# Optimization experiments

Hardware: AMD Instinct MI355X
Metric: run time of the kernel (lower is better)

The kernel has to match this reference:

```python
import jax, jax.numpy as jnp
import numpy as np

B, Q, K, H = 8, 512, 512, 64
KEY_D, QUERY_D, VAL_D = 256, 256, 256

def setup_inputs() -> dict:
    key = jax.random.key(0)
    ks = jax.random.split(key, 6)
    return {
        "key": jax.random.normal(ks[0], (B, K, KEY_D), dtype=jnp.float32),
        "query": jax.random.normal(ks[1], (B, Q, QUERY_D), dtype=jnp.float32),
        "value": jax.random.normal(ks[2], (B, K, VAL_D), dtype=jnp.float32),
        "mask": jnp.zeros((B, Q, K), dtype=bool),
        "W_k": jax.random.normal(ks[3], (KEY_D, H), dtype=jnp.float32) / np.sqrt(KEY_D),
        "W_q": jax.random.normal(ks[4], (QUERY_D, H), dtype=jnp.float32) / np.sqrt(QUERY_D),
        "w_v": jax.random.normal(ks[5], (H,), dtype=jnp.float32) / np.sqrt(H),
    }

def reference(key, query, value, mask, W_k, W_q, w_v):
    q = query @ W_q                      # [B, Q, H]
    k = key @ W_k                        # [B, K, H]
    feats = jnp.tanh(q[:, :, None, :] + k[:, None, :, :])  # [B, Q, K, H]
    score = jnp.einsum('bqkh,h->bqk', feats, w_v)           # [B, Q, K]
    score = jnp.where(mask, -jnp.inf, score)
    attn = jax.nn.softmax(score, axis=-1)                   # [B, Q, K]
    return jnp.einsum('bqk,bkd->bqd', attn, value)          # [B, Q, VAL_D]
```

## Files before the change

### kernel.cpp

```cpp
#include <hip/hip_runtime.h>
#include <math.h>

#define NB 8
#define NQ 512
#define NK 512
#define NH 64
#define ND 256
#define QT 8

typedef float f32x2 __attribute__((ext_vector_type(2)));
typedef float f32x4 __attribute__((ext_vector_type(4)));
typedef _Float16 f16x2 __attribute__((ext_vector_type(2)));
typedef _Float16 f16x8 __attribute__((ext_vector_type(8)));

#define EXP2(x) __builtin_amdgcn_exp2f(x)
#define RCP(x)  __builtin_amdgcn_rcpf(x)
#define SCALE2 2.8853900817779268f
#define LOG2E  1.4426950408889634f

static __device__ __forceinline__ f32x2 sp2(float v) { return (f32x2){v, v}; }
static __device__ __forceinline__ f32x2 fma2(f32x2 a, f32x2 b, f32x2 c) {
    return __builtin_elementwise_fma(a, b, c);
}
static __device__ __forceinline__ f32x2 mk2(float x, float y) {
    return (f32x2){x, y};
}
static __device__ __forceinline__ f16x2 cvt2h(float a, float b) {
#if __has_builtin(__builtin_amdgcn_cvt_pkrtz)
    return __builtin_bit_cast(f16x2, __builtin_amdgcn_cvt_pkrtz(a, b));
#else
    return (f16x2){(_Float16)a, (_Float16)b};
#endif
}

static __device__ __forceinline__ void score4(
    const f32x2 k0, const f32x2 k1, const f32x2 k2, const f32x2 k3,
    const f32x4 eqv, const f32x4 fqv, const float w01a, const float w01b,
    f32x2& acc)
{
    const f32x2 t0 = k0 * eqv.x;
    const f32x2 t1 = k1 * eqv.y;
    const f32x2 ua = t0 + t1 + 1.0f;
    const f32x2 da = fma2(t0, t1, ua);
    f32x2 na = fma2(k0, sp2(fqv.x), sp2(w01a));
    na = fma2(k1, sp2(fqv.y), na);
    const f32x2 t2 = k2 * eqv.z;
    const f32x2 t3 = k3 * eqv.w;
    const f32x2 ub = t2 + t3 + 1.0f;
    const f32x2 db = fma2(t2, t3, ub);
    f32x2 nb = fma2(k2, sp2(fqv.z), sp2(w01b));
    nb = fma2(k3, sp2(fqv.w), nb);
    const f32x2 D = da * db;
    f32x2 N = na * db;
    N = fma2(nb, da, N);
    const f32x2 rD = mk2(RCP(D.x), RCP(D.y));
    acc = fma2(N, rD, acc);
}

__global__ __launch_bounds__(256, 4) void proj_kernel(
    const float* __restrict__ query, const float* __restrict__ key,
    const float* __restrict__ value,
    const float* __restrict__ Wq, const float* __restrict__ Wk,
    const float* __restrict__ w_v,
    float* __restrict__ qside, float* __restrict__ Ekp,
    float* __restrict__ w01g, float* __restrict__ wsumg,
    _Float16* __restrict__ VhT)
{
    const int t = threadIdx.x;

    if (blockIdx.x >= 1024) {
        const int vbase = ((int)blockIdx.x - 1024) * 8;
        const int bb = vbase >> 9, k0 = vbase & 511;
        const int d = t;
        const float* __restrict__ vsrc = value + ((size_t)bb * NK + k0) * ND + d;
        float v[8];
        #pragma unroll
        for (int j = 0; j < 8; ++j) v[j] = vsrc[(size_t)j * ND];
        f16x8 hv;
        #pragma unroll
        for (int j = 0; j < 4; ++j) {
            const f16x2 h = cvt2h(v[2 * j], v[2 * j + 1]);
            hv[2 * j] = h.x; hv[2 * j + 1] = h.y;
        }
        *(f16x8*)&VhT[((size_t)bb * ND + d) * NK + k0] = hv;
        return;
    }

    __shared__ __align__(16) float insT[ND][12];
    __shared__ float pacc[3][4][NH][2];
    const bool isK = blockIdx.x >= 512;
    const float* __restrict__ in = isK ? key : query;
    const float* __restrict__ W  = isK ? Wk : Wq;
    const int rowbase = (blockIdx.x & 511) * 8;

    {
        const int r = t & 7, c = (t >> 3) * 8;
        const float* src = in + (size_t)(rowbase + r) * ND + c;
        const f32x4 v0 = *(const f32x4*)src;
        const f32x4 v1 = *(const f32x4*)(src + 4);
        insT[c + 0][r] = v0.x; insT[c + 1][r] = v0.y;
        insT[c + 2][r] = v0.z; insT[c + 3][r] = v0.w;
        insT[c + 4][r] = v1.x; insT[c + 5][r] = v1.y;
        insT[c + 6][r] = v1.z; insT[c + 7][r] = v1.w;
    }
    __syncthreads();

    const int lane = t & 63;
    const int w    = t >> 6;
    const int d0   = w * 64;

    f32x2 acc[4] = {{0.f,0.f},{0.f,0.f},{0.f,0.f},{0.f,0.f}};
    for (int dd = 0; dd < 64; ++dd) {
        const int d = d0 + dd;
        const float wv = W[(size_t)d * NH + lane];
        const f32x4 rA = *(const f32x4*)&insT[d][0];
        const f32x4 rB = *(const f32x4*)&insT[d][4];
        acc[0] = fma2(mk2(rA.x, rA.y), sp2(wv), acc[0]);
        acc[1] = fma2(mk2(rA.z, rA.w), sp2(wv), acc[1]);
        acc[2] = fma2(mk2(rB.x, rB.y), sp2(wv), acc[2]);
        acc[3] = fma2(mk2(rB.z, rB.w), sp2(wv), acc[3]);
    }
    if (w > 0) {
        #pragma unroll
        for (int rp = 0; rp < 4; ++rp)
            *(f32x2*)&pacc[w - 1][rp][lane][0] = acc[rp];
    }
    __syncthreads();
    if (w == 0) {
        float e[8];
        #pragma unroll
        for (int rp = 0; rp < 4; ++rp) {
            f32x2 a = acc[rp];
            a += *(const f32x2*)&pacc[0][rp][lane][0];
            a += *(const f32x2*)&pacc[1][rp][lane][0];
            a += *(const f32x2*)&pacc[2][rp][lane][0];
            e[2 * rp] = a.x; e[2 * rp + 1] = a.y;
        }
        #pragma unroll
        for (int j = 0; j < 8; ++j) {
            const float x = fminf(fmaxf(e[j] * SCALE2, -30.f), 30.f);
            e[j] = EXP2(x);
        }
        if (!isK) {
            const float wx = w_v[lane ^ 1];
            #pragma unroll
            for (int j = 0; j < 8; ++j) {
                const int g = rowbase + j;
                float* dst = qside + ((size_t)g * 16 + (lane >> 2)) * 8 + (lane & 3);
                dst[0] = e[j];
                dst[4] = wx * e[j];
            }
        } else {
            #pragma unroll
            for (int j = 0; j < 8; ++j) {
                const int g = rowbase + j;
                const int bb = g >> 9, kk = g & 511;
                Ekp[((size_t)bb * NH + lane) * NK + kk] = e[j];
            }
        }
    }
    if (blockIdx.x == 0) {
        if (t < 32) w01g[t] = w_v[2 * t] + w_v[2 * t + 1];
        if (t == 64) {
            float s = 0.f;
            for (int h = 0; h < NH; ++h) s += w_v[h];
            wsumg[0] = s;
        }
    }
}

__global__ __launch_bounds__(512, 4) void score_kernel(
    const float* __restrict__ qside, const float* __restrict__ Ekp,
    const unsigned char* __restrict__ mask,
    const float* __restrict__ w01g, const float* __restrict__ wsumg,
    _Float16* __restrict__ Ph)
{
    __shared__ float reds[QT][4];

    const int t    = threadIdx.x;
    const int lane = t & 63;
    const int w    = t >> 6;
    const int bid  = ((int)(blockIdx.x & 7) << 6) | ((int)blockIdx.x >> 3);
    const int b    = bid >> 6;
    const int q0   = (bid & 63) * QT;
    const int rh   = __builtin_amdgcn_readfirstlane(t >> 8);
    const int kp   = t & 255;

    const float wsumL = wsumg[0] * LOG2E;
    const float* __restrict__ qs  = qside + (size_t)(b * NQ + q0 + rh * 4) * 128;
    const float* __restrict__ ekc = Ekp + (size_t)b * NH * NK + 2 * kp;

    f32x2 eA[4], eB[4];
    #pragma unroll
    for (int j = 0; j < 4; ++j) eA[j] = *(const f32x2*)&ekc[(size_t)j * NK];
    #pragma unroll
    for (int j = 0; j < 4; ++j) eB[j] = *(const f32x2*)&ekc[(size_t)(4 + j) * NK];

    f32x2 acc[4] = {{0.f,0.f},{0.f,0.f},{0.f,0.f},{0.f,0.f}};

    for (int hc = 0; hc < 16; hc += 2) {
        {
            const f32x2 k0 = eA[0], k1 = eA[1], k2 = eA[2], k3 = eA[3];
            if (hc + 2 < 16) {
                #pragma unroll
                for (int j = 0; j < 4; ++j)
                    eA[j] = *(const f32x2*)&ekc[(size_t)(4 * (hc + 2) + j) * NK];
            }
            const float wa = w01g[2 * hc], wb = w01g[2 * hc + 1];
            #pragma unroll
            for (int r = 0; r < 4; ++r) {
                const f32x4 eqv = *(const f32x4*)&qs[r * 128 + hc * 8];
                const f32x4 fqv = *(const f32x4*)&qs[r * 128 + hc * 8 + 4];
                score4(k0, k1, k2, k3, eqv, fqv, wa, wb, acc[r]);
            }
        }
        {
            const f32x2 k0 = eB[0], k1 = eB[1], k2 = eB[2], k3 = eB[3];
            if (hc + 3 < 16) {
                #pragma unroll
                for (int j = 0; j < 4; ++j)
                    eB[j] = *(const f32x2*)&ekc[(size_t)(4 * (hc + 3) + j) * NK];
            }
            const float wa = w01g[2 * hc + 2], wb = w01g[2 * hc + 3];
            #pragma unroll
            for (int r = 0; r < 4; ++r) {
                const f32x4 eqv = *(const f32x4*)&qs[r * 128 + (hc + 1) * 8];
                const f32x4 fqv = *(const f32x4*)&qs[r * 128 + (hc + 1) * 8 + 4];
                score4(k0, k1, k2, k3, eqv, fqv, wa, wb, acc[r]);
            }
        }
    }

    const unsigned char* __restrict__ mb =
        mask + (size_t)(b * NQ + q0 + rh * 4) * NK + 2 * kp;
    f32x2 p[4];
    #pragma unroll
    for (int r = 0; r < 4; ++r) {
        f32x2 arg = fma2(acc[r], sp2(-2.f * LOG2E), sp2(wsumL));
        const unsigned short m = *(const unsigned short*)(mb + (size_t)r * NK);
        if (m & 0x00ff) arg.x = -__builtin_inff();
        if (m & 0xff00) arg.y = -__builtin_inff();
        p[r] = mk2(EXP2(arg.x), EXP2(arg.y));
    }

    #pragma unroll
    for (int r = 0; r < 4; ++r) {
        float s = p[r].x + p[r].y;
        #pragma unroll
        for (int off = 32; off; off >>= 1) s += __shfl_xor(s, off, 64);
        if (lane == 0) reds[rh * 4 + r][w & 3] = s;
    }
    __syncthreads();
    #pragma unroll
    for (int r = 0; r < 4; ++r) {
        const f32x4 sv = *(const f32x4*)&reds[rh * 4 + r][0];
        const float rin = RCP((sv.x + sv.y) + (sv.z + sv.w));
        const f32x2 pn = p[r] * rin;
        *(f16x2*)&Ph[(size_t)(b * NQ + q0 + rh * 4 + r) * NK + 2 * kp] =
            cvt2h(pn.x, pn.y);
    }
}

__global__ __launch_bounds__(512, 4) void pv_kernel(
    const _Float16* __restrict__ Ph, const _Float16* __restrict__ VhT,
    float* __restrict__ out)
{
    const int t    = threadIdx.x;
    const int lane = t & 63;
    const int w    = t >> 6;
    const int bid  = ((int)(blockIdx.x & 7) << 5) | ((int)blockIdx.x >> 3);
    const int b    = bid >> 5;
    const int q0   = (bid & 31) * 16;
    const int ln   = lane & 15;
    const int kg   = lane >> 4;

    const _Float16* __restrict__ pA =
        Ph + (size_t)(b * NQ + q0 + ln) * NK + kg * 8;
    const _Float16* __restrict__ pB0 =
        VhT + (size_t)(b * ND + w * 32 + ln) * NK + kg * 8;
    const _Float16* __restrict__ pB1 = pB0 + (size_t)16 * NK;

    f32x4 c0 = {0.f, 0.f, 0.f, 0.f}, c1 = {0.f, 0.f, 0.f, 0.f};
    f16x8 a  = *(const f16x8*)pA;
    f16x8 b0 = *(const f16x8*)pB0;
    f16x8 b1 = *(const f16x8*)pB1;

    #pragma unroll
    for (int s = 0; s < 16; ++s) {
        f16x8 an = a, b0n = b0, b1n = b1;
        if (s < 15) {
            an  = *(const f16x8*)(pA  + 32 * (s + 1));
            b0n = *(const f16x8*)(pB0 + 32 * (s + 1));
            b1n = *(const f16x8*)(pB1 + 32 * (s + 1));
        }
        c0 = __builtin_amdgcn_mfma_f32_16x16x32_f16(a, b0, c0, 0, 0, 0);
        c1 = __builtin_amdgcn_mfma_f32_16x16x32_f16(a, b1, c1, 0, 0, 0);
        a = an; b0 = b0n; b1 = b1n;
    }

    #pragma unroll
    for (int i = 0; i < 4; ++i) {
        float* __restrict__ o =
            out + (size_t)(b * NQ + q0 + 4 * kg + i) * ND + w * 32 + ln;
        o[0]  = c0[i];
        o[16] = c1[i];
    }
}

extern "C" void kernel_launch(void* const* d_in, const int* in_sizes, int n_in,
                              void* d_out, int out_size, void* d_ws, size_t ws_size,
                              hipStream_t stream) {
    const float* key   = (const float*)d_in[0];
    const float* query = (const float*)d_in[1];
    const float* value = (const float*)d_in[2];
    const unsigned char* mask = (const unsigned char*)d_in[3];
    const float* Wk  = (const float*)d_in[4];
    const float* Wq  = (const float*)d_in[5];
    const float* w_v = (const float*)d_in[6];
    float* out = (float*)d_out;

    float* Ekp   = (float*)d_ws;
    float* qside = Ekp + (size_t)NB * NH * NK;
    float* w01g  = qside + (size_t)NB * NQ * 128;
    float* wsumg = w01g + 32;
    _Float16* Ph  = (_Float16*)(w01g + 64);
    _Float16* VhT = Ph + (size_t)NB * NQ * NK;

    proj_kernel<<<1536, 256, 0, stream>>>(query, key, value, Wq, Wk, w_v,
                                          qside, Ekp, w01g, wsumg, VhT);
    score_kernel<<<512, 512, 0, stream>>>(qside, Ekp, mask, w01g, wsumg, Ph);
    pv_kernel<<<256, 512, 0, stream>>>(Ph, VhT, out);
}
```

Before: 46.44 us.

## Split score kernel over key halves and defer softmax normalization to PV

The score kernel now splits each 8-query tile across two blocks, each covering half the keys with 2 rows per thread group instead of 4, doubling the grid to 1024 blocks. Unnormalized exp values are written to the fp16 probability buffer, and per-half row sums go to a small workspace array. The PV kernel reads both partial sums and scales its output by their reciprocal. This is meant to raise parallelism and occupancy and to remove the post-barrier normalization pass. In exchange, each query row's data is loaded by twice as many blocks, and storing unnormalized values in fp16 risks overflow or lost precision when scores are large.

```diff
diff --git a/kernel.cpp b/kernel.cpp
--- a/kernel.cpp
+++ b/kernel.cpp
@@ -7,6 +7,7 @@
 #define NH 64
 #define ND 256
 #define QT 8
+#define KH 256
 
 typedef float f32x2 __attribute__((ext_vector_type(2)));
 typedef float f32x4 __attribute__((ext_vector_type(4)));
@@ -173,22 +174,25 @@
     const float* __restrict__ qside, const float* __restrict__ Ekp,
     const unsigned char* __restrict__ mask,
     const float* __restrict__ w01g, const float* __restrict__ wsumg,
-    _Float16* __restrict__ Ph)
+    _Float16* __restrict__ Ph, float* __restrict__ sums)
 {
-    __shared__ float reds[QT][4];
+    __shared__ float reds[QT][2];
 
     const int t    = threadIdx.x;
     const int lane = t & 63;
     const int w    = t >> 6;
-    const int bid  = ((int)(blockIdx.x & 7) << 6) | ((int)blockIdx.x >> 3);
-    const int b    = bid >> 6;
-    const int q0   = (bid & 63) * QT;
-    const int rh   = __builtin_amdgcn_readfirstlane(t >> 8);
-    const int kp   = t & 255;
+    const int bid  = ((int)(blockIdx.x & 7) << 7) | ((int)blockIdx.x >> 3);
+    const int b    = bid >> 7;
+    const int rem  = bid & 127;
+    const int q0   = (rem >> 1) * QT;
+    const int half = rem & 1;
+    const int rh   = __builtin_amdgcn_readfirstlane(t >> 7);
+    const int kpl  = t & 127;
+    const int k    = half * KH + 2 * kpl;
 
     const float wsumL = wsumg[0] * LOG2E;
-    const float* __restrict__ qs  = qside + (size_t)(b * NQ + q0 + rh * 4) * 128;
-    const float* __restrict__ ekc = Ekp + (size_t)b * NH * NK + 2 * kp;
+    const float* __restrict__ qs  = qside + (size_t)(b * NQ + q0 + rh * 2) * 128;
+    const float* __restrict__ ekc = Ekp + (size_t)b * NH * NK + k;
 
     f32x2 eA[4], eB[4];
     #pragma unroll
@@ -196,7 +200,7 @@
     #pragma unroll
     for (int j = 0; j < 4; ++j) eB[j] = *(const f32x2*)&ekc[(size_t)(4 + j) * NK];
 
-    f32x2 acc[4] = {{0.f,0.f},{0.f,0.f},{0.f,0.f},{0.f,0.f}};
+    f32x2 acc[2] = {{0.f,0.f},{0.f,0.f}};
 
     for (int hc = 0; hc < 16; hc += 2) {
         {
@@ -208,7 +212,7 @@
             }
             const float wa = w01g[2 * hc], wb = w01g[2 * hc + 1];
             #pragma unroll
-            for (int r = 0; r < 4; ++r) {
+            for (int r = 0; r < 2; ++r) {
                 const f32x4 eqv = *(const f32x4*)&qs[r * 128 + hc * 8];
                 const f32x4 fqv = *(const f32x4*)&qs[r * 128 + hc * 8 + 4];
                 score4(k0, k1, k2, k3, eqv, fqv, wa, wb, acc[r]);
@@ -223,7 +227,7 @@
             }
             const float wa = w01g[2 * hc + 2], wb = w01g[2 * hc + 3];
             #pragma unroll
-            for (int r = 0; r < 4; ++r) {
+            for (int r = 0; r < 2; ++r) {
                 const f32x4 eqv = *(const f32x4*)&qs[r * 128 + (hc + 1) * 8];
                 const f32x4 fqv = *(const f32x4*)&qs[r * 128 + (hc + 1) * 8 + 4];
                 score4(k0, k1, k2, k3, eqv, fqv, wa, wb, acc[r]);
@@ -232,38 +236,40 @@
     }
 
     const unsigned char* __restrict__ mb =
-        mask + (size_t)(b * NQ + q0 + rh * 4) * NK + 2 * kp;
-    f32x2 p[4];
-    #pragma unroll
-    for (int r = 0; r < 4; ++r) {
+        mask + (size_t)(b * NQ + q0 + rh * 2) * NK + k;
+    f32x2 p[2];
+    #pragma unroll
+    for (int r = 0; r < 2; ++r) {
         f32x2 arg = fma2(acc[r], sp2(-2.f * LOG2E), sp2(wsumL));
         const unsigned short m = *(const unsigned short*)(mb + (size_t)r * NK);
         if (m & 0x00ff) arg.x = -__builtin_inff();
         if (m & 0xff00) arg.y = -__builtin_inff();
         p[r] = mk2(EXP2(arg.x), EXP2(arg.y));
-    }
-
-    #pragma unroll
-    for (int r = 0; r < 4; ++r) {
+        *(f16x2*)&Ph[(size_t)(b * NQ + q0 + rh * 2 + r) * NK + k] =
+            cvt2h(p[r].x, p[r].y);
+    }
+
+    #pragma unroll
+    for (int r = 0; r < 2; ++r) {
         float s = p[r].x + p[r].y;
         #pragma unroll
         for (int off = 32; off; off >>= 1) s += __shfl_xor(s, off, 64);
-        if (lane == 0) reds[rh * 4 + r][w & 3] = s;
+        if (lane == 0) reds[rh * 2 + r][w & 1] = s;
     }
     __syncthreads();
-    #pragma unroll
-    for (int r = 0; r < 4; ++r) {
-        const f32x4 sv = *(const f32x4*)&reds[rh * 4 + r][0];
-        const float rin = RCP((sv.x + sv.y) + (sv.z + sv.w));
-        const f32x2 pn = p[r] * rin;
-        *(f16x2*)&Ph[(size_t)(b * NQ + q0 + rh * 4 + r) * NK + 2 * kp] =
-            cvt2h(pn.x, pn.y);
+    if (lane == 0 && (w & 1) == 0) {
+        #pragma unroll
+        for (int r = 0; r < 2; ++r) {
+            const int row = rh * 2 + r;
+            sums[((size_t)half * NB + b) * NQ + q0 + row] =
+                reds[row][0] + reds[row][1];
+        }
     }
 }
 
 __global__ __launch_bounds__(512, 4) void pv_kernel(
     const _Float16* __restrict__ Ph, const _Float16* __restrict__ VhT,
-    float* __restrict__ out)
+    const float* __restrict__ sums, float* __restrict__ out)
 {
     const int t    = threadIdx.x;
     const int lane = t & 63;
@@ -300,10 +306,13 @@
 
     #pragma unroll
     for (int i = 0; i < 4; ++i) {
-        float* __restrict__ o =
-            out + (size_t)(b * NQ + q0 + 4 * kg + i) * ND + w * 32 + ln;
-        o[0]  = c0[i];
-        o[16] = c1[i];
+        const int row = q0 + 4 * kg + i;
+        const float s0 = sums[((size_t)0 * NB + b) * NQ + row];
+        const float s1 = sums[((size_t)1 * NB + b) * NQ + row];
+        const float rs = RCP(s0 + s1);
+        float* __restrict__ o = out + (size_t)(b * NQ + row) * ND + w * 32 + ln;
+        o[0]  = c0[i] * rs;
+        o[16] = c1[i] * rs;
     }
 }
 
@@ -323,11 +332,13 @@
     float* qside = Ekp + (size_t)NB * NH * NK;
     float* w01g  = qside + (size_t)NB * NQ * 128;
     float* wsumg = w01g + 32;
-    _Float16* Ph  = (_Float16*)(w01g + 64);
+    float* sums  = w01g + 64;
+    _Float16* Ph  = (_Float16*)(sums + 2 * NB * NQ);
     _Float16* VhT = Ph + (size_t)NB * NQ * NK;
 
     proj_kernel<<<1536, 256, 0, stream>>>(query, key, value, Wq, Wk, w_v,
                                           qside, Ekp, w01g, wsumg, VhT);
-    score_kernel<<<512, 512, 0, stream>>>(qside, Ekp, mask, w01g, wsumg, Ph);
-    pv_kernel<<<256, 512, 0, stream>>>(Ph, VhT, out);
-}
+    score_kernel<<<NB * 64 * 2, 512, 0, stream>>>(qside, Ekp, mask,
+                                                  w01g, wsumg, Ph, sums);
+    pv_kernel<<<256, 512, 0, stream>>>(Ph, VhT, sums, out);
+}
```

New measurement: 47.56 us (median of 2 runs). 2.4% more time.
